# Kernel optimization log

Hardware: AMD Instinct MI355X
Metric: run time of the kernel (lower is better)

## Reference

```python
import jax, jax.numpy as jnp
import numpy as np

K = 20
EPS = 1e-5
NEG_SLOPE = 0.2


def setup_inputs() -> dict:
    key = jax.random.key(0)
    k1, k2, k3, k4 = jax.random.split(key, 4)
    B, C, N, O = 8, 64, 4096, 64
    x = jax.random.normal(k1, (B, C, N), dtype=jnp.float32)
    # Conv2d(2C, O, kernel_size=1, bias=False) -> weight [O, 2C]
    W = jax.random.normal(k2, (O, 2 * C), dtype=jnp.float32) * (1.0 / np.sqrt(2 * C))
    gamma = jnp.ones((O,), dtype=jnp.float32)
    beta = jnp.zeros((O,), dtype=jnp.float32)
    return {"x": x, "W": W, "gamma": gamma, "beta": beta}


def reference(x, W, gamma, beta):
    B, C, N = x.shape
    xt = jnp.transpose(x, (0, 2, 1))  # [B, N, C]
    # knn: negative squared pairwise distance, topk -> nearest neighbors
    inner = jnp.einsum('bic,bjc->bij', xt, xt)  # [B, N, N]
    xx = jnp.sum(xt * xt, axis=-1)              # [B, N]
    neg_dist = 2.0 * inner - xx[:, :, None] - xx[:, None, :]
    _, idx = jax.lax.top_k(neg_dist, K)         # [B, N, K]
    # gather neighbor features: [B, N, K, C]
    feature = jax.vmap(lambda f, i: f[i])(xt, idx)
    x_central = jnp.broadcast_to(xt[:, :, None, :], (B, N, K, C))
    edge = jnp.concatenate([feature - x_central, x_central], axis=-1)  # [B, N, K, 2C]
    # 1x1 conv == matmul over channel dim
    y = jnp.einsum('bnkc,oc->bnko', edge, W)    # [B, N, K, O]
    # BatchNorm2d in training mode: batch stats over (B, N, K) per channel
    mean = jnp.mean(y, axis=(0, 1, 2))
    var = jnp.var(y, axis=(0, 1, 2))
    y = (y - mean) * jax.lax.rsqrt(var + EPS) * gamma + beta
    y = jnp.where(y >= 0, y, NEG_SLOPE * y)     # LeakyReLU(0.2)
    out = jnp.max(y, axis=2)                    # max over k neighbors -> [B, N, O]
    return jnp.transpose(out, (0, 2, 1))        # [B, O, N]
```

## Files before the change

kernel.cpp:

```cpp
#include <hip/hip_runtime.h>
#include <cstdint>
#include <cstddef>

#define BB 8
#define CC 64
#define NN 4096
#define OO 64
#define KK 20
#define TWO_C 128
#define BN (BB * NN)

#define JCH 128
#define GSPLIT 8
#define GJPB (NN / GSPLIT)
#define CSPLIT 4
#define CJPB (NN / CSPLIT)
#define SEGCAP 32

typedef float vf4 __attribute__((ext_vector_type(4)));
typedef float f4  __attribute__((ext_vector_type(4)));
typedef _Float16 hf2 __attribute__((ext_vector_type(2)));
typedef _Float16 h8  __attribute__((ext_vector_type(8)));

__device__ __forceinline__ unsigned int pack_h2(float a, float b) {
    hf2 h; h.x = (_Float16)a; h.y = (_Float16)b;
    return __builtin_bit_cast(unsigned int, h);
}

__device__ __forceinline__ unsigned int fmap(float d) {
    unsigned int s = __float_as_uint(d);
    return s ^ (unsigned int)(((int)s >> 31) | 0x80000000);
}

__device__ __forceinline__ unsigned long long cmpx(unsigned long long key, int lane, int j, bool dirDesc) {
    unsigned long long o = __shfl_xor(key, j, 64);
    bool lower = (lane & j) == 0;
    bool takeMax = (dirDesc == lower);
    return ((o > key) == takeMax) ? o : key;
}

__global__ __launch_bounds__(256) void transpose_kernel(const float* __restrict__ x,
                                                        float* __restrict__ xT,
                                                        unsigned int* __restrict__ xTh) {
    __shared__ float t[64][65];
    const int b = blockIdx.y;
    const int n0 = blockIdx.x * 64;
    const int tid = threadIdx.x;
    const int ln = tid & 63, g = tid >> 6;
#pragma unroll
    for (int i = 0; i < 16; ++i) {
        int c = g * 16 + i;
        t[c][ln] = x[((size_t)b * CC + c) * NN + n0 + ln];
    }
    __syncthreads();
#pragma unroll
    for (int i = 0; i < 16; ++i) {
        int nl = g * 16 + i;
        xT[((size_t)b * NN + n0 + nl) * CC + ln] = t[ln][nl];
    }
#pragma unroll
    for (int it = 0; it < 8; ++it) {
        int e = it * 256 + tid;
        int nl = e >> 5, cp = e & 31;
        xTh[((size_t)b * NN + n0 + nl) * 32 + cp] = pack_h2(t[2*cp][nl], t[2*cp+1][nl]);
    }
}

__global__ __launch_bounds__(256) void xx_kernel(const float* __restrict__ x,
                                                 float* __restrict__ xx) {
    int t = blockIdx.x * 256 + threadIdx.x;
    int b = t >> 12, n = t & (NN - 1);
    const float* xp = x + (size_t)b * CC * NN + n;
    float acc = 0.f;
#pragma unroll
    for (int c = 0; c < CC; ++c) {
        float v = xp[(size_t)c * NN];
        acc += v * v;
    }
    xx[t] = acc;
}

__global__ __launch_bounds__(256) void knn_gmax_kernel(const unsigned int* __restrict__ xTh,
                                                       const float* __restrict__ xx,
                                                       float* __restrict__ gmaxG) {
    __shared__ unsigned int stage[JCH * 36];
    __shared__ float xxh[JCH];
    const int tid = threadIdx.x;
    const int wv = tid >> 6, lane = tid & 63;
    const int lcol = lane & 15, lrow = lane >> 4;
    const int b = blockIdx.z;
    const int i0 = blockIdx.x * 128;
    const int j0 = blockIdx.y * GJPB;
    const unsigned int* xb = xTh + (size_t)b * NN * 32;
    const float* xxb = xx + (size_t)b * NN;

    const uint4* ap0 = (const uint4*)(xb + (size_t)(i0 + wv * 32 + lcol) * 32 + lrow * 4);
    const uint4* ap1 = (const uint4*)(xb + (size_t)(i0 + wv * 32 + 16 + lcol) * 32 + lrow * 4);
    uint4 A00 = ap0[0], A01 = ap0[4];
    uint4 A10 = ap1[0], A11 = ap1[4];

    float m[8];
#pragma unroll
    for (int s = 0; s < 8; ++s) m[s] = -3.4e38f;

    uint4 pf[4];
    float pxx;
    {
        const uint4* src = (const uint4*)(xb + (size_t)j0 * 32);
#pragma unroll
        for (int gi = 0; gi < 4; ++gi) pf[gi] = src[gi * 256 + tid];
        pxx = xxb[j0 + (tid & 127)];
    }

    int g = j0 >> 7;
    for (int jc = j0; jc < j0 + GJPB; jc += JCH) {
        __syncthreads();
#pragma unroll
        for (int gi = 0; gi < 4; ++gi) {
            int e4 = gi * 256 + tid;
            *(uint4*)&stage[(e4 >> 3) * 36 + (e4 & 7) * 4] = pf[gi];
        }
        if (tid < JCH) xxh[tid] = 0.5f * pxx;
        __syncthreads();
        if (jc + JCH < j0 + GJPB) {
            const uint4* src = (const uint4*)(xb + (size_t)(jc + JCH) * 32);
#pragma unroll
            for (int gi = 0; gi < 4; ++gi) pf[gi] = src[gi * 256 + tid];
            pxx = xxb[jc + JCH + (tid & 127)];
        }
#pragma unroll
        for (int jt = 0; jt < 8; ++jt) {
            const uint4* bp = (const uint4*)&stage[(jt * 16 + lcol) * 36 + lrow * 4];
            uint4 B0 = bp[0], B1 = bp[4];
            f4 acc0 = {0.f, 0.f, 0.f, 0.f};
            f4 acc1 = {0.f, 0.f, 0.f, 0.f};
            acc0 = __builtin_amdgcn_mfma_f32_16x16x32_f16(__builtin_bit_cast(h8, A00), __builtin_bit_cast(h8, B0), acc0, 0, 0, 0);
            acc0 = __builtin_amdgcn_mfma_f32_16x16x32_f16(__builtin_bit_cast(h8, A01), __builtin_bit_cast(h8, B1), acc0, 0, 0, 0);
            acc1 = __builtin_amdgcn_mfma_f32_16x16x32_f16(__builtin_bit_cast(h8, A10), __builtin_bit_cast(h8, B0), acc1, 0, 0, 0);
            acc1 = __builtin_amdgcn_mfma_f32_16x16x32_f16(__builtin_bit_cast(h8, A11), __builtin_bit_cast(h8, B1), acc1, 0, 0, 0);
            float h = xxh[jt * 16 + lcol];
#pragma unroll
            for (int r = 0; r < 4; ++r) {
                m[r]     = fmaxf(m[r],     acc0[r] - h);
                m[4 + r] = fmaxf(m[4 + r], acc1[r] - h);
            }
        }
#pragma unroll
        for (int s = 0; s < 8; ++s) {
#pragma unroll
            for (int off = 1; off < 16; off <<= 1)
                m[s] = fmaxf(m[s], __shfl_xor(m[s], off));
        }
        if (lcol == 0) {
            int r0 = b * NN + i0 + wv * 32 + lrow * 4;
            f4 m0; m0[0] = m[0]; m0[1] = m[1]; m0[2] = m[2]; m0[3] = m[3];
            f4 m1; m1[0] = m[4]; m1[1] = m[5]; m1[2] = m[6]; m1[3] = m[7];
            *(f4*)&gmaxG[(size_t)g * BN + r0]      = m0;
            *(f4*)&gmaxG[(size_t)g * BN + r0 + 16] = m1;
        }
#pragma unroll
        for (int s = 0; s < 8; ++s) m[s] = -3.4e38f;
        ++g;
    }
}

__global__ __launch_bounds__(256) void knn_thresh_kernel(const float* __restrict__ gmaxG,
                                                         float* __restrict__ Tg) {
    const int row = blockIdx.x * 256 + threadIdx.x;
    float L[KK];
#pragma unroll
    for (int s = 0; s < KK; ++s) L[s] = -3.4e38f;
#pragma unroll
    for (int g = 0; g < 32; ++g) {
        float xv = gmaxG[(size_t)g * BN + row];
#pragma unroll
        for (int s = 0; s < KK; ++s) {
            float hi = fmaxf(xv, L[s]);
            xv = fminf(xv, L[s]);
            L[s] = hi;
        }
    }
    Tg[row] = L[KK - 1];
}

__global__ __launch_bounds__(256) void knn_collect_kernel(const unsigned int* __restrict__ xTh,
                                                          const float* __restrict__ xx,
                                                          const float* __restrict__ Tg,
                                                          unsigned short* __restrict__ cand,
                                                          unsigned int* __restrict__ cntS) {
    __shared__ unsigned int stage[JCH * 36];
    __shared__ float xxh[JCH];
    __shared__ unsigned short bufL[128][SEGCAP];
    __shared__ unsigned int cntL[128];
    const int tid = threadIdx.x;
    const int wv = tid >> 6, lane = tid & 63;
    const int lcol = lane & 15, lrow = lane >> 4;
    const int b = blockIdx.z;
    const int i0 = blockIdx.x * 128;
    const int seg = blockIdx.y;
    const int j0 = seg * CJPB;
    const unsigned int* xb = xTh + (size_t)b * NN * 32;
    const float* xxb = xx + (size_t)b * NN;

    if (tid < 128) cntL[tid] = 0;

    const uint4* ap0 = (const uint4*)(xb + (size_t)(i0 + wv * 32 + lcol) * 32 + lrow * 4);
    const uint4* ap1 = (const uint4*)(xb + (size_t)(i0 + wv * 32 + 16 + lcol) * 32 + lrow * 4);
    uint4 A00 = ap0[0], A01 = ap0[4];
    uint4 A10 = ap1[0], A11 = ap1[4];

    const int rl0 = wv * 32 + lrow * 4;
    const int gr0 = b * NN + i0 + rl0;
    f4 t0 = *(const f4*)&Tg[gr0];
    f4 t1 = *(const f4*)&Tg[gr0 + 16];

    uint4 pf[4];
    float pxx;
    {
        const uint4* src = (const uint4*)(xb + (size_t)j0 * 32);
#pragma unroll
        for (int gi = 0; gi < 4; ++gi) pf[gi] = src[gi * 256 + tid];
        pxx = xxb[j0 + (tid & 127)];
    }

    for (int jc = j0; jc < j0 + CJPB; jc += JCH) {
        __syncthreads();
#pragma unroll
        for (int gi = 0; gi < 4; ++gi) {
            int e4 = gi * 256 + tid;
            *(uint4*)&stage[(e4 >> 3) * 36 + (e4 & 7) * 4] = pf[gi];
        }
        if (tid < JCH) xxh[tid] = 0.5f * pxx;
        __syncthreads();
        if (jc + JCH < j0 + CJPB) {
            const uint4* src = (const uint4*)(xb + (size_t)(jc + JCH) * 32);
#pragma unroll
            for (int gi = 0; gi < 4; ++gi) pf[gi] = src[gi * 256 + tid];
            pxx = xxb[jc + JCH + (tid & 127)];
        }
#pragma unroll
        for (int jt = 0; jt < 8; ++jt) {
            const uint4* bp = (const uint4*)&stage[(jt * 16 + lcol) * 36 + lrow * 4];
            uint4 B0 = bp[0], B1 = bp[4];
            f4 acc0 = {0.f, 0.f, 0.f, 0.f};
            f4 acc1 = {0.f, 0.f, 0.f, 0.f};
            acc0 = __builtin_amdgcn_mfma_f32_16x16x32_f16(__builtin_bit_cast(h8, A00), __builtin_bit_cast(h8, B0), acc0, 0, 0, 0);
            acc0 = __builtin_amdgcn_mfma_f32_16x16x32_f16(__builtin_bit_cast(h8, A01), __builtin_bit_cast(h8, B1), acc0, 0, 0, 0);
            acc1 = __builtin_amdgcn_mfma_f32_16x16x32_f16(__builtin_bit_cast(h8, A10), __builtin_bit_cast(h8, B0), acc1, 0, 0, 0);
            acc1 = __builtin_amdgcn_mfma_f32_16x16x32_f16(__builtin_bit_cast(h8, A11), __builtin_bit_cast(h8, B1), acc1, 0, 0, 0);
            float h = xxh[jt * 16 + lcol];
            const int jj = jc + jt * 16 + lcol;
#pragma unroll
            for (int r = 0; r < 4; ++r) {
                if (acc0[r] - h >= t0[r]) {
                    unsigned int s = atomicAdd(&cntL[rl0 + r], 1u);
                    if (s < SEGCAP) bufL[rl0 + r][s] = (unsigned short)jj;
                }
                if (acc1[r] - h >= t1[r]) {
                    unsigned int s = atomicAdd(&cntL[rl0 + 16 + r], 1u);
                    if (s < SEGCAP) bufL[rl0 + 16 + r][s] = (unsigned short)jj;
                }
            }
        }
    }
    __syncthreads();
    const unsigned int* bl = (const unsigned int*)&bufL[0][0];
    unsigned int* cd = (unsigned int*)(cand + ((size_t)seg * BN + b * NN + i0) * SEGCAP);
#pragma unroll
    for (int e = tid; e < 128 * SEGCAP / 2; e += 256) cd[e] = bl[e];
    if (tid < 128) cntS[(size_t)seg * BN + b * NN + i0 + tid] = cntL[tid];
}

__global__ __launch_bounds__(256) void knn_merge_kernel(const float* __restrict__ xT,
                                                        const float* __restrict__ xx,
                                                        const unsigned short* __restrict__ cand,
                                                        const unsigned int* __restrict__ cntS,
                                                        unsigned short* __restrict__ idx_out) {
    const int tid = threadIdx.x;
    const int wv = tid >> 6, lane = tid & 63;
    const int rr = __builtin_amdgcn_readfirstlane(blockIdx.x * 4 + wv);
    const int b = rr >> 12, i = rr & (NN - 1);
    const float* xTb = xT + (size_t)b * NN * CC;
    const float* xxb = xx + b * NN;

    vf4 xiv[CC / 4];
    const float* xip = xTb + (size_t)i * CC;
#pragma unroll
    for (int c4 = 0; c4 < CC / 4; ++c4) xiv[c4] = *(const vf4*)(xip + 4 * c4);

    const unsigned int c0 = cntS[(size_t)0 * BN + rr];
    const unsigned int c1 = cntS[(size_t)1 * BN + rr];
    const unsigned int c2 = cntS[(size_t)2 * BN + rr];
    const unsigned int c3 = cntS[(size_t)3 * BN + rr];
    const bool segovf = (c0 > SEGCAP) || (c1 > SEGCAP) || (c2 > SEGCAP) || (c3 > SEGCAP);
    const unsigned int p1 = c0, p2 = c0 + c1, p3 = c0 + c1 + c2, total = p3 + c3;

    auto dot_key = [&](int jj) -> unsigned long long {
        const float* xj = xTb + (size_t)jj * CC;
        float a0 = 0.f, a1 = 0.f, a2 = 0.f, a3 = 0.f;
#pragma unroll
        for (int c4 = 0; c4 < CC / 4; ++c4) {
            vf4 xjv = *(const vf4*)(xj + 4 * c4);
            a0 = fmaf(xiv[c4].x, xjv.x, a0);
            a1 = fmaf(xiv[c4].y, xjv.y, a1);
            a2 = fmaf(xiv[c4].z, xjv.z, a2);
            a3 = fmaf(xiv[c4].w, xjv.w, a3);
        }
        float d = 2.f * ((a0 + a1) + (a2 + a3)) - xxb[jj];
        return ((unsigned long long)fmap(d) << 32) | (unsigned int)(NN - 1 - jj);
    };

    auto fetch_key = [&](unsigned int l) -> unsigned long long {
        if (l >= total) return 0ull;
        int jj;
        if (l < p1)      jj = cand[((size_t)0 * BN + rr) * SEGCAP + l];
        else if (l < p2) jj = cand[((size_t)1 * BN + rr) * SEGCAP + (l - p1)];
        else if (l < p3) jj = cand[((size_t)2 * BN + rr) * SEGCAP + (l - p2)];
        else             jj = cand[((size_t)3 * BN + rr) * SEGCAP + (l - p3)];
        return dot_key(jj);
    };

    unsigned long long kout;
    if (!segovf && total <= 64) {
        unsigned long long key = fetch_key((unsigned int)lane);
#pragma unroll
        for (int k = 2; k <= 64; k <<= 1) {
            bool dir = (lane & k) == 0;
#pragma unroll
            for (int j = k >> 1; j > 0; j >>= 1) key = cmpx(key, lane, j, dir);
        }
        kout = key;
    } else if (!segovf) {
        unsigned long long key  = fetch_key((unsigned int)lane);
        unsigned long long key2 = fetch_key((unsigned int)lane + 64);
#pragma unroll
        for (int k = 2; k <= 64; k <<= 1) {
            bool dir0 = (lane & k) == 0;
            bool dir1 = (k == 64) ? false : dir0;
#pragma unroll
            for (int j = k >> 1; j > 0; j >>= 1) {
                key  = cmpx(key,  lane, j, dir0);
                key2 = cmpx(key2, lane, j, dir1);
            }
        }
        {
            unsigned long long mx = key2 > key ? key2 : key;
            unsigned long long mn = key2 > key ? key : key2;
            key = mx; key2 = mn;
        }
#pragma unroll
        for (int j = 32; j > 0; j >>= 1) {
            key  = cmpx(key,  lane, j, true);
            key2 = cmpx(key2, lane, j, true);
        }
        kout = key;
    } else {
        unsigned long long run = 0ull;
        for (int t = 0; t < NN / 64; ++t) {
            unsigned long long key = dot_key(t * 64 + lane);
#pragma unroll
            for (int k = 2; k <= 64; k <<= 1) {
                bool dir = (lane & k) == 0;
#pragma unroll
                for (int j = k >> 1; j > 0; j >>= 1) key = cmpx(key, lane, j, dir);
            }
            unsigned long long rev = __shfl(run, 63 - lane, 64);
            key = key > rev ? key : rev;
#pragma unroll
            for (int j = 32; j > 0; j >>= 1) key = cmpx(key, lane, j, true);
            run = key;
        }
        kout = run;
    }

    if (lane < KK)
        idx_out[(size_t)rr * KK + lane] =
            (unsigned short)(NN - 1 - (unsigned int)(kout & 0xFFFFFFFFull));
}

__global__ __launch_bounds__(256) void pd_kernel(const float* __restrict__ x,
                                                 const float* __restrict__ W,
                                                 float* __restrict__ P,
                                                 float* __restrict__ Dd) {
    __shared__ float w1T[CC][32];
    __shared__ float wdT[CC][32];
    const int tid = threadIdx.x;
    const int b = blockIdx.y;
    const int o0 = blockIdx.z * 32;
    for (int e = tid; e < 32 * CC; e += 256) {
        int ol = e >> 6, c = e & 63;
        float w1 = W[(o0 + ol) * TWO_C + c];
        float w2 = W[(o0 + ol) * TWO_C + CC + c];
        w1T[c][ol] = w1;
        wdT[c][ol] = w2 - w1;
    }
    __syncthreads();
    const int n = blockIdx.x * 256 + tid;
    float accp[32], accd[32];
#pragma unroll
    for (int i = 0; i < 32; ++i) { accp[i] = 0.f; accd[i] = 0.f; }
    const float* xp = x + (size_t)b * CC * NN + n;
    for (int c = 0; c < CC; ++c) {
        float xv = xp[(size_t)c * NN];
        const float4* w1r = (const float4*)&w1T[c][0];
        const float4* wdr = (const float4*)&wdT[c][0];
#pragma unroll
        for (int g = 0; g < 8; ++g) {
            float4 aw = w1r[g]; float4 bw = wdr[g];
            accp[4*g+0] += xv * aw.x; accp[4*g+1] += xv * aw.y;
            accp[4*g+2] += xv * aw.z; accp[4*g+3] += xv * aw.w;
            accd[4*g+0] += xv * bw.x; accd[4*g+1] += xv * bw.y;
            accd[4*g+2] += xv * bw.z; accd[4*g+3] += xv * bw.w;
        }
    }
    size_t base = ((size_t)b * NN + n) * OO + o0;
#pragma unroll
    for (int g = 0; g < 8; ++g) {
        *(float4*)&P[base + 4*g]  = make_float4(accp[4*g], accp[4*g+1], accp[4*g+2], accp[4*g+3]);
        *(float4*)&Dd[base + 4*g] = make_float4(accd[4*g], accd[4*g+1], accd[4*g+2], accd[4*g+3]);
    }
}

__global__ __launch_bounds__(256) void stats_kernel(const float* __restrict__ P,
                                                    const float* __restrict__ Dd,
                                                    const unsigned short* __restrict__ idx,
                                                    double* __restrict__ partials) {
    const int tid = threadIdx.x;
    const int o = tid & 63, g = tid >> 6;
    const int row0 = blockIdx.x * 32;
    double s1 = 0.0, s2 = 0.0;
    for (int i = 0; i < 8; ++i) {
        int row = row0 + g + 4 * i;
        int b = row >> 12;
        float d = Dd[(size_t)row * OO + o];
        const unsigned short* ip = idx + (size_t)row * KK;
        const float* Pb = P + ((size_t)b * NN) * OO;
#pragma unroll
        for (int k = 0; k < KK; ++k) {
            int j = ip[k];
            float y = Pb[(size_t)j * OO + o] + d;
            s1 += (double)y;
            s2 += (double)y * (double)y;
        }
    }
    __shared__ double r1[4][64];
    __shared__ double r2[4][64];
    r1[g][o] = s1; r2[g][o] = s2;
    __syncthreads();
    if (g == 0) {
        double a1 = r1[0][o] + r1[1][o] + r1[2][o] + r1[3][o];
        double a2 = r2[0][o] + r2[1][o] + r2[2][o] + r2[3][o];
        partials[(size_t)blockIdx.x * 128 + o]      = a1;
        partials[(size_t)blockIdx.x * 128 + 64 + o] = a2;
    }
}

#define NSTATB (BB * NN / 32)
__global__ void finalize_kernel(const double* __restrict__ partials,
                                const float* __restrict__ gamma,
                                const float* __restrict__ beta,
                                float* __restrict__ ss) {
    int o = threadIdx.x;
    double s1 = 0.0, s2 = 0.0;
    for (int blk = 0; blk < NSTATB; ++blk) {
        s1 += partials[(size_t)blk * 128 + o];
        s2 += partials[(size_t)blk * 128 + 64 + o];
    }
    const double cnt = (double)BB * NN * KK;
    double mean = s1 / cnt;
    double var = s2 / cnt - mean * mean;
    double rs = 1.0 / sqrt(var + 1e-5);
    double sc = (double)gamma[o] * rs;
    ss[o] = (float)sc;
    ss[64 + o] = (float)((double)beta[o] - mean * sc);
}

__global__ __launch_bounds__(256) void out_kernel(const float* __restrict__ P,
                                                  const float* __restrict__ Dd,
                                                  const unsigned short* __restrict__ idx,
                                                  const float* __restrict__ ss,
                                                  float* __restrict__ out) {
    __shared__ float tile[32][65];
    const int tid = threadIdx.x;
    const int o = tid & 63, g = tid >> 6;
    const int b = blockIdx.y;
    const int n0 = blockIdx.x * 32;
    const float sc = ss[o], sh = ss[64 + o];
    const float* Pb = P + ((size_t)b * NN) * OO;
    for (int i = 0; i < 8; ++i) {
        int nl = g + 4 * i;
        int row = b * NN + n0 + nl;
        float d = Dd[(size_t)row * OO + o];
        const unsigned short* ip = idx + (size_t)row * KK;
        float mv = -__builtin_inff();
#pragma unroll
        for (int k = 0; k < KK; ++k) {
            int j = ip[k];
            float y = Pb[(size_t)j * OO + o] + d;
            float t = y * sc + sh;
            t = (t >= 0.f) ? t : 0.2f * t;
            mv = fmaxf(mv, t);
        }
        tile[nl][o] = mv;
    }
    __syncthreads();
    const int nn = tid & 31, og = tid >> 5;
    for (int i = 0; i < 8; ++i) {
        int oo = og + 8 * i;
        out[((size_t)b * OO + oo) * NN + n0 + nn] = tile[nn][oo];
    }
}

extern "C" void kernel_launch(void* const* d_in, const int* in_sizes, int n_in,
                              void* d_out, int out_size, void* d_ws, size_t ws_size,
                              hipStream_t stream) {
    (void)in_sizes; (void)n_in; (void)out_size; (void)ws_size;
    const float* x     = (const float*)d_in[0];
    const float* W     = (const float*)d_in[1];
    const float* gamma = (const float*)d_in[2];
    const float* beta  = (const float*)d_in[3];
    float* out = (float*)d_out;

    char* ws = (char*)d_ws;
    float*          xx       = (float*)ws;
    float*          xT       = (float*)(ws + 131072);
    unsigned int*   xTh      = (unsigned int*)(ws + 8519680);
    float*          gmaxG    = (float*)(ws + 12713984);
    unsigned short* cand     = (unsigned short*)(ws + 12713984);
    float*          Tg       = (float*)(ws + 21102592);
    unsigned int*   cntS     = (unsigned int*)(ws + 21233664);
    unsigned short* idx      = (unsigned short*)(ws + 8519680);
    float*          P        = (float*)(ws + 131072);
    float*          Dd       = (float*)(ws + 12713984);
    double*         partials = (double*)(ws + 21102592);
    float*          ss       = (float*)(ws + 22151168);

    transpose_kernel<<<dim3(NN / 64, BB), 256, 0, stream>>>(x, xT, xTh);
    xx_kernel<<<dim3(BB * NN / 256), 256, 0, stream>>>(x, xx);
    knn_gmax_kernel<<<dim3(NN / 128, GSPLIT, BB), 256, 0, stream>>>(xTh, xx, gmaxG);
    knn_thresh_kernel<<<dim3(BN / 256), 256, 0, stream>>>(gmaxG, Tg);
    knn_collect_kernel<<<dim3(NN / 128, CSPLIT, BB), 256, 0, stream>>>(xTh, xx, Tg, cand, cntS);
    knn_merge_kernel<<<dim3(BN / 4), 256, 0, stream>>>(xT, xx, cand, cntS, idx);
    pd_kernel<<<dim3(NN / 256, BB, 2), 256, 0, stream>>>(x, W, P, Dd);
    stats_kernel<<<dim3(BN / 32), 256, 0, stream>>>(P, Dd, idx, partials);
    finalize_kernel<<<1, 64, 0, stream>>>(partials, gamma, beta, ss);
    out_kernel<<<dim3(NN / 32, BB), 256, 0, stream>>>(P, Dd, idx, ss, out);
}
```

Baseline: 344.1 us.

## Drop LDS staging in kNN kernels, widen per-wave row tile, split collect finer

The gmax and collect kernels no longer stage the j-tile through shared memory with block barriers. Each wave now loads B fragments directly from global memory (relying on L2/L1 reuse) and covers 64 rows instead of 32, so each B load feeds more MFMAs. The collect pass is split into 8 segments with a 16-slot cap instead of 4 with 32, and the merge kernel is generalised to loop over the segment count. This trades barrier and LDS traffic for more global loads and a smaller per-segment capacity, which raises the risk of overflow fallbacks.

```diff
diff --git a/kernel.cpp b/kernel.cpp
--- a/kernel.cpp
+++ b/kernel.cpp
@@ -10,12 +10,11 @@
 #define TWO_C 128
 #define BN (BB * NN)
 
-#define JCH 128
 #define GSPLIT 8
 #define GJPB (NN / GSPLIT)
-#define CSPLIT 4
+#define CSPLIT 8
 #define CJPB (NN / CSPLIT)
-#define SEGCAP 32
+#define SEGCAP 16
 
 typedef float vf4 __attribute__((ext_vector_type(4)));
 typedef float f4  __attribute__((ext_vector_type(4)));
@@ -83,84 +82,57 @@
 __global__ __launch_bounds__(256) void knn_gmax_kernel(const unsigned int* __restrict__ xTh,
                                                        const float* __restrict__ xx,
                                                        float* __restrict__ gmaxG) {
-    __shared__ unsigned int stage[JCH * 36];
-    __shared__ float xxh[JCH];
     const int tid = threadIdx.x;
     const int wv = tid >> 6, lane = tid & 63;
     const int lcol = lane & 15, lrow = lane >> 4;
     const int b = blockIdx.z;
-    const int i0 = blockIdx.x * 128;
+    const int i0w = blockIdx.x * 256 + wv * 64;
     const int j0 = blockIdx.y * GJPB;
     const unsigned int* xb = xTh + (size_t)b * NN * 32;
     const float* xxb = xx + (size_t)b * NN;
 
-    const uint4* ap0 = (const uint4*)(xb + (size_t)(i0 + wv * 32 + lcol) * 32 + lrow * 4);
-    const uint4* ap1 = (const uint4*)(xb + (size_t)(i0 + wv * 32 + 16 + lcol) * 32 + lrow * 4);
-    uint4 A00 = ap0[0], A01 = ap0[4];
-    uint4 A10 = ap1[0], A11 = ap1[4];
-
-    float m[8];
-#pragma unroll
-    for (int s = 0; s < 8; ++s) m[s] = -3.4e38f;
-
-    uint4 pf[4];
-    float pxx;
-    {
-        const uint4* src = (const uint4*)(xb + (size_t)j0 * 32);
-#pragma unroll
-        for (int gi = 0; gi < 4; ++gi) pf[gi] = src[gi * 256 + tid];
-        pxx = xxb[j0 + (tid & 127)];
+    uint4 A0[4], A1[4];
+#pragma unroll
+    for (int s = 0; s < 4; ++s) {
+        const uint4* ap = (const uint4*)(xb + (size_t)(i0w + s * 16 + lcol) * 32 + lrow * 4);
+        A0[s] = ap[0]; A1[s] = ap[4];
     }
 
     int g = j0 >> 7;
-    for (int jc = j0; jc < j0 + GJPB; jc += JCH) {
-        __syncthreads();
-#pragma unroll
-        for (int gi = 0; gi < 4; ++gi) {
-            int e4 = gi * 256 + tid;
-            *(uint4*)&stage[(e4 >> 3) * 36 + (e4 & 7) * 4] = pf[gi];
-        }
-        if (tid < JCH) xxh[tid] = 0.5f * pxx;
-        __syncthreads();
-        if (jc + JCH < j0 + GJPB) {
-            const uint4* src = (const uint4*)(xb + (size_t)(jc + JCH) * 32);
-#pragma unroll
-            for (int gi = 0; gi < 4; ++gi) pf[gi] = src[gi * 256 + tid];
-            pxx = xxb[jc + JCH + (tid & 127)];
-        }
+    for (int gg = 0; gg < GJPB / 128; ++gg, ++g) {
+        float m[16];
+#pragma unroll
+        for (int s = 0; s < 16; ++s) m[s] = -3.4e38f;
 #pragma unroll
         for (int jt = 0; jt < 8; ++jt) {
-            const uint4* bp = (const uint4*)&stage[(jt * 16 + lcol) * 36 + lrow * 4];
+            const int jj = j0 + gg * 128 + jt * 16 + lcol;
+            const uint4* bp = (const uint4*)(xb + (size_t)jj * 32 + lrow * 4);
             uint4 B0 = bp[0], B1 = bp[4];
-            f4 acc0 = {0.f, 0.f, 0.f, 0.f};
-            f4 acc1 = {0.f, 0.f, 0.f, 0.f};
-            acc0 = __builtin_amdgcn_mfma_f32_16x16x32_f16(__builtin_bit_cast(h8, A00), __builtin_bit_cast(h8, B0), acc0, 0, 0, 0);
-            acc0 = __builtin_amdgcn_mfma_f32_16x16x32_f16(__builtin_bit_cast(h8, A01), __builtin_bit_cast(h8, B1), acc0, 0, 0, 0);
-            acc1 = __builtin_amdgcn_mfma_f32_16x16x32_f16(__builtin_bit_cast(h8, A10), __builtin_bit_cast(h8, B0), acc1, 0, 0, 0);
-            acc1 = __builtin_amdgcn_mfma_f32_16x16x32_f16(__builtin_bit_cast(h8, A11), __builtin_bit_cast(h8, B1), acc1, 0, 0, 0);
-            float h = xxh[jt * 16 + lcol];
-#pragma unroll
-            for (int r = 0; r < 4; ++r) {
-                m[r]     = fmaxf(m[r],     acc0[r] - h);
-                m[4 + r] = fmaxf(m[4 + r], acc1[r] - h);
+            float h = 0.5f * xxb[jj];
+#pragma unroll
+            for (int s = 0; s < 4; ++s) {
+                f4 acc = {0.f, 0.f, 0.f, 0.f};
+                acc = __builtin_amdgcn_mfma_f32_16x16x32_f16(__builtin_bit_cast(h8, A0[s]), __builtin_bit_cast(h8, B0), acc, 0, 0, 0);
+                acc = __builtin_amdgcn_mfma_f32_16x16x32_f16(__builtin_bit_cast(h8, A1[s]), __builtin_bit_cast(h8, B1), acc, 0, 0, 0);
+#pragma unroll
+                for (int r = 0; r < 4; ++r)
+                    m[s * 4 + r] = fmaxf(m[s * 4 + r], acc[r] - h);
             }
         }
 #pragma unroll
-        for (int s = 0; s < 8; ++s) {
+        for (int s = 0; s < 16; ++s) {
 #pragma unroll
             for (int off = 1; off < 16; off <<= 1)
                 m[s] = fmaxf(m[s], __shfl_xor(m[s], off));
         }
         if (lcol == 0) {
-            int r0 = b * NN + i0 + wv * 32 + lrow * 4;
-            f4 m0; m0[0] = m[0]; m0[1] = m[1]; m0[2] = m[2]; m0[3] = m[3];
-            f4 m1; m1[0] = m[4]; m1[1] = m[5]; m1[2] = m[6]; m1[3] = m[7];
-            *(f4*)&gmaxG[(size_t)g * BN + r0]      = m0;
-            *(f4*)&gmaxG[(size_t)g * BN + r0 + 16] = m1;
-        }
-#pragma unroll
-        for (int s = 0; s < 8; ++s) m[s] = -3.4e38f;
-        ++g;
+            int r0 = b * NN + i0w + lrow * 4;
+#pragma unroll
+            for (int s = 0; s < 4; ++s) {
+                f4 mv; mv[0] = m[4*s]; mv[1] = m[4*s+1]; mv[2] = m[4*s+2]; mv[3] = m[4*s+3];
+                *(f4*)&gmaxG[(size_t)g * BN + r0 + s * 16] = mv;
+            }
+        }
     }
 }
 
@@ -188,77 +160,48 @@
                                                           const float* __restrict__ Tg,
                                                           unsigned short* __restrict__ cand,
                                                           unsigned int* __restrict__ cntS) {
-    __shared__ unsigned int stage[JCH * 36];
-    __shared__ float xxh[JCH];
-    __shared__ unsigned short bufL[128][SEGCAP];
-    __shared__ unsigned int cntL[128];
+    __shared__ unsigned short bufL[256][SEGCAP];
+    __shared__ unsigned int cntL[256];
     const int tid = threadIdx.x;
     const int wv = tid >> 6, lane = tid & 63;
     const int lcol = lane & 15, lrow = lane >> 4;
     const int b = blockIdx.z;
-    const int i0 = blockIdx.x * 128;
+    const int i0 = blockIdx.x * 256;
+    const int i0w = i0 + wv * 64;
     const int seg = blockIdx.y;
     const int j0 = seg * CJPB;
     const unsigned int* xb = xTh + (size_t)b * NN * 32;
     const float* xxb = xx + (size_t)b * NN;
 
-    if (tid < 128) cntL[tid] = 0;
-
-    const uint4* ap0 = (const uint4*)(xb + (size_t)(i0 + wv * 32 + lcol) * 32 + lrow * 4);
-    const uint4* ap1 = (const uint4*)(xb + (size_t)(i0 + wv * 32 + 16 + lcol) * 32 + lrow * 4);
-    uint4 A00 = ap0[0], A01 = ap0[4];
-    uint4 A10 = ap1[0], A11 = ap1[4];
-
-    const int rl0 = wv * 32 + lrow * 4;
-    const int gr0 = b * NN + i0 + rl0;
-    f4 t0 = *(const f4*)&Tg[gr0];
-    f4 t1 = *(const f4*)&Tg[gr0 + 16];
-
-    uint4 pf[4];
-    float pxx;
-    {
-        const uint4* src = (const uint4*)(xb + (size_t)j0 * 32);
-#pragma unroll
-        for (int gi = 0; gi < 4; ++gi) pf[gi] = src[gi * 256 + tid];
-        pxx = xxb[j0 + (tid & 127)];
-    }
-
-    for (int jc = j0; jc < j0 + CJPB; jc += JCH) {
-        __syncthreads();
-#pragma unroll
-        for (int gi = 0; gi < 4; ++gi) {
-            int e4 = gi * 256 + tid;
-            *(uint4*)&stage[(e4 >> 3) * 36 + (e4 & 7) * 4] = pf[gi];
-        }
-        if (tid < JCH) xxh[tid] = 0.5f * pxx;
-        __syncthreads();
-        if (jc + JCH < j0 + CJPB) {
-            const uint4* src = (const uint4*)(xb + (size_t)(jc + JCH) * 32);
-#pragma unroll
-            for (int gi = 0; gi < 4; ++gi) pf[gi] = src[gi * 256 + tid];
-            pxx = xxb[jc + JCH + (tid & 127)];
-        }
-#pragma unroll
-        for (int jt = 0; jt < 8; ++jt) {
-            const uint4* bp = (const uint4*)&stage[(jt * 16 + lcol) * 36 + lrow * 4];
-            uint4 B0 = bp[0], B1 = bp[4];
-            f4 acc0 = {0.f, 0.f, 0.f, 0.f};
-            f4 acc1 = {0.f, 0.f, 0.f, 0.f};
-            acc0 = __builtin_amdgcn_mfma_f32_16x16x32_f16(__builtin_bit_cast(h8, A00), __builtin_bit_cast(h8, B0), acc0, 0, 0, 0);
-            acc0 = __builtin_amdgcn_mfma_f32_16x16x32_f16(__builtin_bit_cast(h8, A01), __builtin_bit_cast(h8, B1), acc0, 0, 0, 0);
-            acc1 = __builtin_amdgcn_mfma_f32_16x16x32_f16(__builtin_bit_cast(h8, A10), __builtin_bit_cast(h8, B0), acc1, 0, 0, 0);
-            acc1 = __builtin_amdgcn_mfma_f32_16x16x32_f16(__builtin_bit_cast(h8, A11), __builtin_bit_cast(h8, B1), acc1, 0, 0, 0);
-            float h = xxh[jt * 16 + lcol];
-            const int jj = jc + jt * 16 + lcol;
+    cntL[tid] = 0;
+    __syncthreads();
+
+    uint4 A0[4], A1[4];
+    f4 tt[4];
+#pragma unroll
+    for (int s = 0; s < 4; ++s) {
+        const uint4* ap = (const uint4*)(xb + (size_t)(i0w + s * 16 + lcol) * 32 + lrow * 4);
+        A0[s] = ap[0]; A1[s] = ap[4];
+        tt[s] = *(const f4*)&Tg[b * NN + i0w + s * 16 + lrow * 4];
+    }
+
+#pragma unroll 4
+    for (int jt = 0; jt < CJPB / 16; ++jt) {
+        const int jj = j0 + jt * 16 + lcol;
+        const uint4* bp = (const uint4*)(xb + (size_t)jj * 32 + lrow * 4);
+        uint4 B0 = bp[0], B1 = bp[4];
+        float h = 0.5f * xxb[jj];
+#pragma unroll
+        for (int s = 0; s < 4; ++s) {
+            f4 acc = {0.f, 0.f, 0.f, 0.f};
+            acc = __builtin_amdgcn_mfma_f32_16x16x32_f16(__builtin_bit_cast(h8, A0[s]), __builtin_bit_cast(h8, B0), acc, 0, 0, 0);
+            acc = __builtin_amdgcn_mfma_f32_16x16x32_f16(__builtin_bit_cast(h8, A1[s]), __builtin_bit_cast(h8, B1), acc, 0, 0, 0);
 #pragma unroll
             for (int r = 0; r < 4; ++r) {
-                if (acc0[r] - h >= t0[r]) {
-                    unsigned int s = atomicAdd(&cntL[rl0 + r], 1u);
-                    if (s < SEGCAP) bufL[rl0 + r][s] = (unsigned short)jj;
-                }
-                if (acc1[r] - h >= t1[r]) {
-                    unsigned int s = atomicAdd(&cntL[rl0 + 16 + r], 1u);
-                    if (s < SEGCAP) bufL[rl0 + 16 + r][s] = (unsigned short)jj;
+                if (acc[r] - h >= tt[s][r]) {
+                    int rl = wv * 64 + s * 16 + lrow * 4 + r;
+                    unsigned int slot = atomicAdd(&cntL[rl], 1u);
+                    if (slot < SEGCAP) bufL[rl][slot] = (unsigned short)jj;
                 }
             }
         }
@@ -267,8 +210,8 @@
     const unsigned int* bl = (const unsigned int*)&bufL[0][0];
     unsigned int* cd = (unsigned int*)(cand + ((size_t)seg * BN + b * NN + i0) * SEGCAP);
 #pragma unroll
-    for (int e = tid; e < 128 * SEGCAP / 2; e += 256) cd[e] = bl[e];
-    if (tid < 128) cntS[(size_t)seg * BN + b * NN + i0 + tid] = cntL[tid];
+    for (int e = tid; e < 256 * SEGCAP / 2; e += 256) cd[e] = bl[e];
+    cntS[(size_t)seg * BN + b * NN + i0 + tid] = cntL[tid];
 }
 
 __global__ __launch_bounds__(256) void knn_merge_kernel(const float* __restrict__ xT,
@@ -288,12 +231,15 @@
 #pragma unroll
     for (int c4 = 0; c4 < CC / 4; ++c4) xiv[c4] = *(const vf4*)(xip + 4 * c4);
 
-    const unsigned int c0 = cntS[(size_t)0 * BN + rr];
-    const unsigned int c1 = cntS[(size_t)1 * BN + rr];
-    const unsigned int c2 = cntS[(size_t)2 * BN + rr];
-    const unsigned int c3 = cntS[(size_t)3 * BN + rr];
-    const bool segovf = (c0 > SEGCAP) || (c1 > SEGCAP) || (c2 > SEGCAP) || (c3 > SEGCAP);
-    const unsigned int p1 = c0, p2 = c0 + c1, p3 = c0 + c1 + c2, total = p3 + c3;
+    unsigned int cs[CSPLIT];
+    bool segovf = false;
+    unsigned int total = 0;
+#pragma unroll
+    for (int s = 0; s < CSPLIT; ++s) {
+        cs[s] = cntS[(size_t)s * BN + rr];
+        segovf |= (cs[s] > SEGCAP);
+        total += cs[s];
+    }
 
     auto dot_key = [&](int jj) -> unsigned long long {
         const float* xj = xTb + (size_t)jj * CC;
@@ -312,11 +258,14 @@
 
     auto fetch_key = [&](unsigned int l) -> unsigned long long {
         if (l >= total) return 0ull;
-        int jj;
-        if (l < p1)      jj = cand[((size_t)0 * BN + rr) * SEGCAP + l];
-        else if (l < p2) jj = cand[((size_t)1 * BN + rr) * SEGCAP + (l - p1)];
-        else if (l < p3) jj = cand[((size_t)2 * BN + rr) * SEGCAP + (l - p2)];
-        else             jj = cand[((size_t)3 * BN + rr) * SEGCAP + (l - p3)];
+        int jj = 0;
+        unsigned int base = 0;
+#pragma unroll
+        for (int s = 0; s < CSPLIT; ++s) {
+            if (l >= base && l < base + cs[s])
+                jj = cand[((size_t)s * BN + rr) * SEGCAP + (l - base)];
+            base += cs[s];
+        }
         return dot_key(jj);
     };
 
@@ -533,13 +482,13 @@
     float*          P        = (float*)(ws + 131072);
     float*          Dd       = (float*)(ws + 12713984);
     double*         partials = (double*)(ws + 21102592);
-    float*          ss       = (float*)(ws + 22151168);
+    float*          ss       = (float*)(ws + 22282240);
 
     transpose_kernel<<<dim3(NN / 64, BB), 256, 0, stream>>>(x, xT, xTh);
     xx_kernel<<<dim3(BB * NN / 256), 256, 0, stream>>>(x, xx);
-    knn_gmax_kernel<<<dim3(NN / 128, GSPLIT, BB), 256, 0, stream>>>(xTh, xx, gmaxG);
+    knn_gmax_kernel<<<dim3(NN / 256, GSPLIT, BB), 256, 0, stream>>>(xTh, xx, gmaxG);
     knn_thresh_kernel<<<dim3(BN / 256), 256, 0, stream>>>(gmaxG, Tg);
-    knn_collect_kernel<<<dim3(NN / 128, CSPLIT, BB), 256, 0, stream>>>(xTh, xx, Tg, cand, cntS);
+    knn_collect_kernel<<<dim3(NN / 256, CSPLIT, BB), 256, 0, stream>>>(xTh, xx, Tg, cand, cntS);
     knn_merge_kernel<<<dim3(BN / 4), 256, 0, stream>>>(xT, xx, cand, cntS, idx);
     pd_kernel<<<dim3(NN / 256, BB, 2), 256, 0, stream>>>(x, W, P, Dd);
     stats_kernel<<<dim3(BN / 32), 256, 0, stream>>>(P, Dd, idx, partials);
```

Measured after the change: 449.4 us. 30.6% more time.
